# Kernel tuning notes

Measured on AMD Instinct MI355X. Metric: run time of the kernel, lower is better.

Reference implementation:

```python
import jax, jax.numpy as jnp
import numpy as np

B, C, H, W = 8, 128, 64, 64
NWIN, HEADS, QKDIM, KVPW, TOPK = 8, 8, 128, 4, 16
SCALE = QKDIM ** -0.5

def _ln(x, g, b, eps):
    mu = x.mean(-1, keepdims=True)
    var = ((x - mu) ** 2).mean(-1, keepdims=True)
    return (x - mu) * jax.lax.rsqrt(var + eps) * g + b

def _conv(x, w, b, pad, groups=1):
    y = jax.lax.conv_general_dilated(x, w, (1, 1), [(pad, pad), (pad, pad)],
        dimension_numbers=('NCHW', 'OIHW', 'NCHW'), feature_group_count=groups)
    return y + b[None, :, None, None]

def setup_inputs():
    key = jax.random.key(0)
    ks = jax.random.split(key, 8)
    s = 0.05
    return {
        't1': jax.random.normal(ks[0], (B, C, H, W), jnp.float32),
        't2': jax.random.normal(ks[1], (B, C, H, W), jnp.float32),
        'pos_w': jax.random.normal(ks[2], (C, 1, 3, 3), jnp.float32) * s,
        'pos_b': jnp.zeros((C,), jnp.float32),
        'cat_w': jax.random.normal(ks[3], (C, 2 * C, 3, 3), jnp.float32) * s,
        'cat_b': jnp.zeros((C,), jnp.float32),
        'ln_cat_g': jnp.ones((C,), jnp.float32),
        'ln_cat_b': jnp.zeros((C,), jnp.float32),
        'ln1_g': jnp.ones((C,), jnp.float32),
        'ln1_b': jnp.zeros((C,), jnp.float32),
        'qkv_w': jax.random.normal(ks[4], (2 * QKDIM + C, C), jnp.float32) * s,
        'qkv_b': jnp.zeros((2 * QKDIM + C,), jnp.float32),
        'lepe_w': jax.random.normal(ks[5], (C, 1, 5, 5), jnp.float32) * s,
        'lepe_b': jnp.zeros((C,), jnp.float32),
        'wo_w': jax.random.normal(ks[6], (C, C), jnp.float32) * s,
        'wo_b': jnp.zeros((C,), jnp.float32),
    }

def _bra_cross(q_in, kv_in, qkv_w, qkv_b, lepe_w, lepe_b, wo_w, wo_b):
    # Bi-level routing cross attention: queries from q_in, keys/values from kv_in (NHWC).
    p = NWIN; wh, ww = H // p, W // p; p2 = p * p
    q = (q_in @ qkv_w.T + qkv_b)[..., :QKDIM]          # (B,H,W,QKDIM)
    kv = (kv_in @ qkv_w.T + qkv_b)[..., QKDIM:]        # (B,H,W,QKDIM+C)

    def win(x):
        c = x.shape[-1]
        return x.reshape(B, p, wh, p, ww, c).transpose(0, 1, 3, 2, 4, 5).reshape(B, p2, wh, ww, c)

    qw, kvw = win(q), win(kv)
    q_pix = qw.reshape(B, p2, wh * ww, QKDIM)
    # adaptive avg-pool each window's kv to KVPW x KVPW ('ada_avgpool')
    f = wh // KVPW
    kv_pix = kvw.reshape(B, p2, KVPW, f, KVPW, f, QKDIM + C).mean(axis=(3, 5))
    kv_pix = kv_pix.reshape(B, p2, KVPW * KVPW, QKDIM + C)
    q_win = qw.mean(axis=(2, 3))                        # (B,p2,QKDIM)
    k_win = kvw[..., :QKDIM].mean(axis=(2, 3))
    # LePE: depthwise 5x5 conv on full-resolution v
    v_full = kv[..., QKDIM:].transpose(0, 3, 1, 2)
    lepe = _conv(v_full, lepe_w, lepe_b, 2, groups=C).transpose(0, 2, 3, 1)
    # region-level routing (detached: diff_routing=False)
    logits = jnp.einsum('bpc,bqc->bpq',
                        jax.lax.stop_gradient(q_win) * SCALE,
                        jax.lax.stop_gradient(k_win))
    _, r_idx = jax.lax.top_k(logits, TOPK)              # (B,p2,TOPK)
    # gather kv of routed regions: (B,p2,TOPK,KVPW^2,QKDIM+C)
    kv_sel = jax.vmap(lambda kvp, idx: kvp[idx])(kv_pix, r_idx)
    k_sel = kv_sel[..., :QKDIM].reshape(B, p2, TOPK * KVPW * KVPW, HEADS, QKDIM // HEADS)
    v_sel = kv_sel[..., QKDIM:].reshape(B, p2, TOPK * KVPW * KVPW, HEADS, C // HEADS)
    q_h = q_pix.reshape(B, p2, wh * ww, HEADS, QKDIM // HEADS)
    attn = jnp.einsum('bpqmc,bpkmc->bpmqk', q_h * SCALE, k_sel)
    attn = jax.nn.softmax(attn, axis=-1)
    out = jnp.einsum('bpmqk,bpkmc->bpqmc', attn, v_sel).reshape(B, p2, wh, ww, C)
    out = out.reshape(B, p, p, wh, ww, C).transpose(0, 1, 3, 2, 4, 5).reshape(B, H, W, C)
    out = out + lepe
    return out @ wo_w.T + wo_b

def reference(t1, t2, pos_w, pos_b, cat_w, cat_b, ln_cat_g, ln_cat_b,
              ln1_g, ln1_b, qkv_w, qkv_b, lepe_w, lepe_b, wo_w, wo_b):
    # Block.forward: depthwise conv positional embedding
    t1 = t1 + _conv(t1, pos_w, pos_b, 1, groups=C)
    t2 = t2 + _conv(t2, pos_w, pos_b, 1, groups=C)
    t1n = t1.transpose(0, 2, 3, 1)
    t2n = t2.transpose(0, 2, 3, 1)
    # RGBConcatConv: cat on channel-last, 3x3 conv, relu(LayerNorm)
    xc = jnp.concatenate([t1n, t2n], axis=3).transpose(0, 3, 1, 2)
    xc = _conv(xc, cat_w, cat_b, 1).transpose(0, 2, 3, 1)
    x = jax.nn.relu(_ln(xc, ln_cat_g, ln_cat_b, 1e-5))
    attn = _bra_cross(_ln(t1n, ln1_g, ln1_b, 1e-6), _ln(t2n, ln1_g, ln1_b, 1e-6),
                      qkv_w, qkv_b, lepe_w, lepe_b, wo_w, wo_b)
    x = x + attn
    return x.transpose(0, 3, 1, 2)
```

## Files before the change

kernel.cpp:

```cpp
#include <hip/hip_runtime.h>
#include <math.h>

typedef unsigned short ushort_t;
typedef __attribute__((ext_vector_type(4))) float f32x4;
typedef __attribute__((ext_vector_type(16))) float f32x16;
typedef __attribute__((ext_vector_type(8))) short bf16x8;

constexpr int B = 8, C = 128, H = 64, W = 64;
constexpr int HEADS = 8, TOPK = 16;
constexpr int P2 = 64;
constexpr float SCALE = 0.0883883476483184405f;

constexpr size_t NPIX    = (size_t)B * H * W;
constexpr size_t OFF_T1C = 0;
constexpr size_t OFF_T2C = OFF_T1C + NPIX * 128;
constexpr size_t OFF_X   = OFF_T2C + NPIX * 128;
constexpr size_t OFF_QB  = OFF_X   + NPIX * 128;
constexpr size_t OFF_KV  = OFF_QB  + NPIX * 64;
constexpr size_t OFF_KVP = OFF_KV  + NPIX * 256;
constexpr size_t OFF_RW1 = OFF_KVP + 524288;
constexpr size_t OFF_RW2 = OFF_RW1 + 524288;
constexpr size_t OFF_KVPT= OFF_KVP + (size_t)B * P2 * 16 * 256;
constexpr size_t OFF_QW  = OFF_KVPT+ (size_t)B * P2 * 128 * 16 / 2;
constexpr size_t OFF_KW  = OFF_QW  + (size_t)B * P2 * 128;
constexpr size_t OFF_RIDX= OFF_KW  + (size_t)B * P2 * 128;
constexpr size_t OFF_WCB = OFF_RIDX+ (size_t)B * P2 * TOPK;
constexpr size_t OFF_QKVB= OFF_WCB + (size_t)9 * 256 * 128;
constexpr size_t OFF_WOB = OFF_QKVB+ (size_t)384 * 128 / 2;
constexpr size_t OFF_T1B = OFF_WOB + 8192;
constexpr size_t OFF_T2B = OFF_T1B + NPIX * 64;

__device__ inline ushort_t f2bf(float f) {
    unsigned u = __float_as_uint(f);
    unsigned r = u + 0x7FFFu + ((u >> 16) & 1u);
    return (ushort_t)(r >> 16);
}
__device__ inline float bf2f(ushort_t u) {
    return __uint_as_float((unsigned)u << 16);
}

__global__ __launch_bounds__(256) void prep_pos_k(
        const float* __restrict__ t1, const float* __restrict__ t2,
        const float* __restrict__ pos_w, const float* __restrict__ pos_b,
        const float* __restrict__ qkv_w, const float* __restrict__ wo_w,
        const float* __restrict__ cat_w,
        ushort_t* __restrict__ qkvB, ushort_t* __restrict__ woB,
        ushort_t* __restrict__ wcat2,
        float* __restrict__ out1, float* __restrict__ out2,
        ushort_t* __restrict__ ob1, ushort_t* __restrict__ ob2) {
    __shared__ float tile[4][32][33];
    int bid = blockIdx.x;
    int t = threadIdx.x;
    if (bid < 1152) {
        int idx = bid * 256 + t;
        if (idx < 384 * 128) qkvB[idx] = f2bf(qkv_w[idx]);
        if (idx < 128 * 128) woB[idx]  = f2bf(wo_w[idx]);
        if (idx < 36 * 8 * 128 * 8) {
            int i  = idx & 7;
            int n  = (idx >> 3) & 127;
            int r  = idx >> 10;
            int lg = r & 3;
            int kk = (r >> 2) & 1;
            int sdd = r >> 3;
            int dd = sdd % 9, q = sdd / 9;
            int ci = q * 64 + kk * 32 + lg * 8 + i;
            wcat2[idx] = f2bf(cat_w[((size_t)n * 256 + ci) * 9 + dd]);
        }
        return;
    }
    int pb = bid - 1152;
    int xb = pb & 1, cg = (pb >> 1) & 3, z = pb >> 3;
    int which = z >> 7, rem = z & 127;
    int b = rem >> 4, y0 = (rem & 15) * 4;
    const float* in = which ? t2 : t1;
    float* outNHWC = which ? out2 : out1;
    ushort_t* outB = which ? ob2 : ob1;
    int c0 = cg * 32, x0 = xb * 32;
    int tx = t & 31, tg = t >> 5;
    int x = x0 + tx;
    for (int i = 0; i < 4; i++) {
        int cl = tg * 4 + i, c = c0 + cl;
        const float* base = in + (size_t)(b * C + c) * H * W;
        float wv[9];
#pragma unroll
        for (int j = 0; j < 9; j++) wv[j] = pos_w[c * 9 + j];
        float rows[6][3];
#pragma unroll
        for (int yy = 0; yy < 6; yy++) {
            int gy = y0 - 1 + yy;
            bool yok = (gy >= 0 && gy < H);
#pragma unroll
            for (int dx = 0; dx < 3; dx++) {
                int gx = x + dx - 1;
                rows[yy][dx] = (yok && gx >= 0 && gx < W) ? base[gy * W + gx] : 0.f;
            }
        }
        float bb = pos_b[c];
#pragma unroll
        for (int k = 0; k < 4; k++) {
            float acc = rows[k + 1][1] + bb;
#pragma unroll
            for (int dy = 0; dy < 3; dy++)
#pragma unroll
                for (int dx = 0; dx < 3; dx++)
                    acc += rows[k + dy][dx] * wv[dy * 3 + dx];
            tile[k][cl][tx] = acc;
        }
    }
    __syncthreads();
    for (int k = 0; k < 4; k++)
        for (int i = 0; i < 4; i++) {
            int xl = tg * 4 + i;
            float val = tile[k][tx][xl];
            size_t idx = ((size_t)(b * H + y0 + k) * W + x0 + xl) * 128 + c0 + tx;
            outNHWC[idx] = val;
            outB[idx] = f2bf(val);
        }
}

constexpr int HALO_B2 = 180 * 144;
constexpr int XSH_B   = 128 * 272;
__global__ __launch_bounds__(512) void cat_ln_k(
        const ushort_t* __restrict__ t1b, const ushort_t* __restrict__ t2b,
        const ushort_t* __restrict__ wcat2,
        const float* __restrict__ cat_b,
        const float* __restrict__ gcat, const float* __restrict__ bcat,
        ushort_t* __restrict__ xbuf,
        const float* __restrict__ t1c, const float* __restrict__ t2c,
        const float* __restrict__ g1, const float* __restrict__ b1,
        const ushort_t* __restrict__ qkvB, const float* __restrict__ qkv_b,
        ushort_t* __restrict__ outQ, ushort_t* __restrict__ outKV,
        float* __restrict__ rw1, float* __restrict__ rw2) {
    __shared__ __align__(16) unsigned char smem[XSH_B + 8192];
    int bid = blockIdx.x;
    int t = threadIdx.x;
    int lane = t & 63, wv = t >> 6;
    int l15 = lane & 15, lg = lane >> 4;

    if (bid < 256) {
        int cb = bid;
        int mw = wv >> 2, nw = wv & 3;
        int b = cb >> 5, y0 = ((cb >> 3) & 3) * 16, x0 = (cb & 7) * 8;

        f32x4 acc[4][2];
#pragma unroll
        for (int mt = 0; mt < 4; mt++)
#pragma unroll
            for (int cf = 0; cf < 2; cf++)
                acc[mt][cf] = (f32x4){0.f, 0.f, 0.f, 0.f};

        int pyA[4], pxA[4];
#pragma unroll
        for (int mt = 0; mt < 4; mt++) {
            int p = mw * 64 + mt * 16 + l15;
            pyA[mt] = p >> 3; pxA[mt] = p & 7;
        }

        for (int q = 0; q < 4; q++) {
            __syncthreads();
            {
                const ushort_t* src = (q < 2 ? t1b : t2b);
                int coff = (q & 1) * 64;
                for (int e = t; e < 1440; e += 512) {
                    int pix = e >> 3, c8 = e & 7;
                    int hy = pix / 10, hx = pix - hy * 10;
                    int gy = y0 - 1 + hy, gx = x0 - 1 + hx;
                    uint4 v = make_uint4(0u, 0u, 0u, 0u);
                    if (gy >= 0 && gy < H && gx >= 0 && gx < W)
                        v = *reinterpret_cast<const uint4*>(
                            src + ((size_t)(b * H + gy) * W + gx) * 128 + coff + c8 * 8);
                    *reinterpret_cast<uint4*>(smem + pix * 144 + c8 * 16) = v;
                }
            }
            __syncthreads();
#pragma unroll
            for (int dd = 0; dd < 9; dd++) {
                int dy = dd / 3, dx = dd - dy * 3;
                const ushort_t* wb = wcat2 + ((size_t)((q * 9 + dd) * 8 + lg) * 128) * 8;
                bf16x8 bfr[2][2];
#pragma unroll
                for (int kk = 0; kk < 2; kk++)
#pragma unroll
                    for (int cf = 0; cf < 2; cf++)
                        bfr[kk][cf] = *reinterpret_cast<const bf16x8*>(
                            wb + (size_t)kk * 4096 + (nw * 32 + cf * 16 + l15) * 8);
#pragma unroll
                for (int mt = 0; mt < 4; mt++) {
                    bf16x8 af[2];
#pragma unroll
                    for (int kk = 0; kk < 2; kk++)
                        af[kk] = *reinterpret_cast<const bf16x8*>(
                            smem + ((pyA[mt] + dy) * 10 + pxA[mt] + dx) * 144 +
                            kk * 64 + lg * 16);
#pragma unroll
                    for (int cf = 0; cf < 2; cf++)
#pragma unroll
                        for (int kk = 0; kk < 2; kk++)
                            acc[mt][cf] = __builtin_amdgcn_mfma_f32_16x16x32_bf16(
                                af[kk], bfr[kk][cf], acc[mt][cf], 0, 0, 0);
                }
            }
        }

        ushort_t* xsh = (ushort_t*)smem;
        float* psum  = (float*)(smem + XSH_B);
        float* psum2 = (float*)(smem + XSH_B + 4096);
        float gv[2], bvv[2];
#pragma unroll
        for (int cf = 0; cf < 2; cf++) {
            int n = nw * 32 + cf * 16 + l15;
            float cbv = cat_b[n];
            gv[cf] = gcat[n]; bvv[cf] = bcat[n];
#pragma unroll
            for (int mt = 0; mt < 4; mt++)
#pragma unroll
                for (int i = 0; i < 4; i++) acc[mt][cf][i] += cbv;
        }
#pragma unroll
        for (int mt = 0; mt < 4; mt++)
#pragma unroll
            for (int i = 0; i < 4; i++) {
                float s = acc[mt][0][i] + acc[mt][1][i];
                float s2 = acc[mt][0][i] * acc[mt][0][i] + acc[mt][1][i] * acc[mt][1][i];
                s  += __shfl_xor(s, 1, 64);  s2 += __shfl_xor(s2, 1, 64);
                s  += __shfl_xor(s, 2, 64);  s2 += __shfl_xor(s2, 2, 64);
                s  += __shfl_xor(s, 4, 64);  s2 += __shfl_xor(s2, 4, 64);
                s  += __shfl_xor(s, 8, 64);  s2 += __shfl_xor(s2, 8, 64);
                int p = mw * 64 + mt * 16 + lg * 4 + i;
                if (l15 == 0) { psum[wv * 128 + p] = s; psum2[wv * 128 + p] = s2; }
            }
        __syncthreads();
#pragma unroll
        for (int mt = 0; mt < 4; mt++)
#pragma unroll
            for (int i = 0; i < 4; i++) {
                int p = mw * 64 + mt * 16 + lg * 4 + i;
                float tot = 0.f, tot2 = 0.f;
#pragma unroll
                for (int j = 0; j < 4; j++) {
                    tot  += psum[(mw * 4 + j) * 128 + p];
                    tot2 += psum2[(mw * 4 + j) * 128 + p];
                }
                float mean = tot * (1.f / 128.f);
                float inv = rsqrtf(tot2 * (1.f / 128.f) - mean * mean + 1e-5f);
#pragma unroll
                for (int cf = 0; cf < 2; cf++) {
                    float v = (acc[mt][cf][i] - mean) * inv * gv[cf] + bvv[cf];
                    xsh[p * 136 + nw * 32 + cf * 16 + l15] = f2bf(fmaxf(v, 0.f));
                }
            }
        __syncthreads();
        for (int e = t; e < 2048; e += 512) {
            int pix = e >> 4, c16 = e & 15;
            int gy = y0 + (pix >> 3), gx = x0 + (pix & 7);
            *reinterpret_cast<uint4*>(
                xbuf + ((size_t)(b * H + gy) * W + gx) * 128 + c16 * 8) =
                *reinterpret_cast<const uint4*>(xsh + pix * 136 + c16 * 8);
        }
        return;
    }

    unsigned char* ash = smem;
    int lb = bid - 256;
    int which = lb >> 8;
    int blk = lb & 255;
    const float* in = which ? t2c : t1c;
    float* rw = which ? rw2 : rw1;
    size_t p0 = (size_t)blk * 128;
    int bb_ = blk >> 5, y0 = (blk & 31) * 2;
    {
        int row = t >> 2, sub = t & 3;
        const float* src = in + (p0 + row) * 128 + sub * 32;
        float4 v[8];
        float s = 0.f;
#pragma unroll
        for (int j = 0; j < 8; j++) {
            v[j] = *reinterpret_cast<const float4*>(src + j * 4);
            s += v[j].x + v[j].y + v[j].z + v[j].w;
        }
        s += __shfl_xor(s, 1, 64); s += __shfl_xor(s, 2, 64);
        float mean = s * (1.f / 128.f);
        float s2 = 0.f;
#pragma unroll
        for (int j = 0; j < 8; j++) {
            float dx = v[j].x - mean, dy = v[j].y - mean;
            float dz = v[j].z - mean, dw = v[j].w - mean;
            s2 += dx * dx + dy * dy + dz * dz + dw * dw;
        }
        s2 += __shfl_xor(s2, 1, 64); s2 += __shfl_xor(s2, 2, 64);
        float inv = rsqrtf(s2 * (1.f / 128.f) + 1e-6f);
        int wj = (wv & 3) * 2 + (lane >> 5);
        int yy_ = y0 + (wv >> 2);
        bool writer = (lane & 28) == 0;
        float* rwp = rw + (((size_t)(bb_ * 8 + wj) * 64 + yy_) * 128) + sub * 32;
#pragma unroll
        for (int j = 0; j < 8; j++) {
            int c = sub * 32 + j * 4;
            float4 gv = *reinterpret_cast<const float4*>(g1 + c);
            float4 bv = *reinterpret_cast<const float4*>(b1 + c);
            float o0 = (v[j].x - mean) * inv * gv.x + bv.x;
            float o1 = (v[j].y - mean) * inv * gv.y + bv.y;
            float o2 = (v[j].z - mean) * inv * gv.z + bv.z;
            float o3 = (v[j].w - mean) * inv * gv.w + bv.w;
            uint2 pk;
            pk.x = (unsigned)f2bf(o0) | ((unsigned)f2bf(o1) << 16);
            pk.y = (unsigned)f2bf(o2) | ((unsigned)f2bf(o3) << 16);
            *reinterpret_cast<uint2*>(ash + row * 272 + c * 2) = pk;
            float r0 = o0, r1 = o1, r2 = o2, r3 = o3;
#pragma unroll
            for (int m = 4; m <= 16; m <<= 1) {
                r0 += __shfl_xor(r0, m, 64);
                r1 += __shfl_xor(r1, m, 64);
                r2 += __shfl_xor(r2, m, 64);
                r3 += __shfl_xor(r3, m, 64);
            }
            if (writer)
                *reinterpret_cast<float4*>(rwp + j * 4) = make_float4(r0, r1, r2, r3);
        }
    }
    __syncthreads();
    int mh = wv >> 2, nw = wv & 3;
    if (which == 0) {
        f32x4 acc[4][2];
#pragma unroll
        for (int mt = 0; mt < 4; mt++)
#pragma unroll
            for (int nn = 0; nn < 2; nn++)
                acc[mt][nn] = (f32x4){0.f, 0.f, 0.f, 0.f};
#pragma unroll
        for (int ks = 0; ks < 4; ks++) {
            bf16x8 af[4];
#pragma unroll
            for (int mt = 0; mt < 4; mt++)
                af[mt] = *reinterpret_cast<const bf16x8*>(
                    ash + (mh * 64 + mt * 16 + l15) * 272 + ks * 64 + lg * 16);
#pragma unroll
            for (int nn = 0; nn < 2; nn++) {
                int n = (nw * 2 + nn) * 16 + l15;
                bf16x8 bfr = *reinterpret_cast<const bf16x8*>(
                    qkvB + (size_t)n * 128 + ks * 32 + lg * 8);
#pragma unroll
                for (int mt = 0; mt < 4; mt++)
                    acc[mt][nn] = __builtin_amdgcn_mfma_f32_16x16x32_bf16(
                        af[mt], bfr, acc[mt][nn], 0, 0, 0);
            }
        }
#pragma unroll
        for (int nn = 0; nn < 2; nn++) {
            int cg = (nw * 2 + nn) * 16 + l15;
            float bv = qkv_b[cg];
#pragma unroll
            for (int mt = 0; mt < 4; mt++)
#pragma unroll
                for (int i = 0; i < 4; i++) {
                    size_t pix = p0 + mh * 64 + mt * 16 + lg * 4 + i;
                    outQ[pix * 128 + cg] = f2bf((acc[mt][nn][i] + bv) * SCALE);
                }
        }
    } else {
        f32x4 acc[4][4];
#pragma unroll
        for (int mt = 0; mt < 4; mt++)
#pragma unroll
            for (int nn = 0; nn < 4; nn++)
                acc[mt][nn] = (f32x4){0.f, 0.f, 0.f, 0.f};
#pragma unroll
        for (int ks = 0; ks < 4; ks++) {
            bf16x8 af[4];
#pragma unroll
            for (int mt = 0; mt < 4; mt++)
                af[mt] = *reinterpret_cast<const bf16x8*>(
                    ash + (mh * 64 + mt * 16 + l15) * 272 + ks * 64 + lg * 16);
#pragma unroll
            for (int nn = 0; nn < 4; nn++) {
                int n = 128 + (nw * 4 + nn) * 16 + l15;
                bf16x8 bfr = *reinterpret_cast<const bf16x8*>(
                    qkvB + (size_t)n * 128 + ks * 32 + lg * 8);
#pragma unroll
                for (int mt = 0; mt < 4; mt++)
                    acc[mt][nn] = __builtin_amdgcn_mfma_f32_16x16x32_bf16(
                        af[mt], bfr, acc[mt][nn], 0, 0, 0);
            }
        }
#pragma unroll
        for (int nn = 0; nn < 4; nn++) {
            int cg = (nw * 4 + nn) * 16 + l15;
            float bv = qkv_b[128 + cg];
#pragma unroll
            for (int mt = 0; mt < 4; mt++)
#pragma unroll
                for (int i = 0; i < 4; i++) {
                    size_t pix = p0 + mh * 64 + mt * 16 + lg * 4 + i;
                    outKV[pix * 256 + cg] = f2bf(acc[mt][nn][i] + bv);
                }
        }
    }
}

__global__ __launch_bounds__(256) void route_pool_k(
        const float* __restrict__ rw1, const float* __restrict__ rw2,
        const float* __restrict__ qkv_w, const float* __restrict__ qkv_b,
        float* __restrict__ qwin, float* __restrict__ kwin,
        const ushort_t* __restrict__ kv,
        ushort_t* __restrict__ kb, ushort_t* __restrict__ kvpT,
        ushort_t* __restrict__ vpl) {
    __shared__ float msh[2][8][128];
    int bid = blockIdx.x;
    int t = threadIdx.x;
    if (bid < 64) {
        int b = bid >> 3, wi = bid & 7;
        for (int i = t; i < 8 * 128; i += 256) {
            int r = i >> 7, c = i & 127;
            size_t off = (((size_t)(b * 8 + r) * 64) + wi * 8) * 128 + c;
            float s1 = 0.f, s2 = 0.f;
#pragma unroll
            for (int rr = 0; rr < 8; rr++) {
                s1 += rw1[off + rr * 128];
                s2 += rw2[off + rr * 128];
            }
            msh[0][r][c] = s1 * (1.f / 64.f);
            msh[1][r][c] = s2 * (1.f / 64.f);
        }
        __syncthreads();
        int c = t;
        int which = c >> 7;
        const float* wrow = qkv_w + (size_t)c * 128;
        float acc[8];
#pragma unroll
        for (int r = 0; r < 8; r++) acc[r] = 0.f;
        for (int k = 0; k < 128; k++) {
            float wv_ = wrow[k];
#pragma unroll
            for (int r = 0; r < 8; r++) acc[r] += msh[which][r][k] * wv_;
        }
        float bv = qkv_b[c];
#pragma unroll
        for (int r = 0; r < 8; r++) {
            size_t o = ((size_t)b * 64 + wi * 8 + r) * 128 + (c & 127);
            (which ? kwin : qwin)[o] = acc[r] + bv;
        }
        return;
    }
    int pb = bid - 64;
    int b = pb >> 6, wdw = pb & 63;
    int wi = wdw >> 3, wj = wdw & 7;
    if (t < 128) {
        float vals[16];
        for (int ry = 0; ry < 4; ry++)
            for (int rx = 0; rx < 4; rx++) {
                float s = 0.f;
                for (int fy = 0; fy < 2; fy++)
                    for (int fx = 0; fx < 2; fx++) {
                        int y = wi * 8 + ry * 2 + fy, x = wj * 8 + rx * 2 + fx;
                        s += bf2f(kv[((size_t)(b * H + y) * W + x) * 256 + t]);
                    }
                vals[ry * 4 + rx] = s * 0.25f;
            }
#pragma unroll
        for (int pos = 0; pos < 16; pos++)
            kb[(((size_t)(b * 64 + wdw)) * 16 + pos) * 128 + t] = f2bf(vals[pos]);
    } else {
        int c = t - 128;
        float ps[4][4];
#pragma unroll
        for (int i = 0; i < 4; i++)
#pragma unroll
            for (int j = 0; j < 4; j++) ps[i][j] = 0.f;
        for (int y = 0; y < 8; y++) {
            union { ushort_t u16[8]; uint4 u4; } raw;
#pragma unroll
            for (int x = 0; x < 8; x++) {
                raw.u16[x] = kv[((size_t)(b * H + wi * 8 + y) * W + wj * 8 + x) * 256 + 128 + c];
                ps[y >> 1][x >> 1] += bf2f(raw.u16[x]);
            }
            *reinterpret_cast<uint4*>(
                vpl + ((size_t)(b * C + c) * H + wi * 8 + y) * W + wj * 8) = raw.u4;
        }
        union { ushort_t u16[16]; uint4 u4[2]; } pk;
#pragma unroll
        for (int ry = 0; ry < 4; ry++)
#pragma unroll
            for (int rx = 0; rx < 4; rx++)
                pk.u16[ry * 4 + rx] = f2bf(ps[ry][rx] * 0.25f);
        size_t base = (((size_t)(b * 64 + wdw)) * 128 + c) * 16;
        *reinterpret_cast<uint4*>(kvpT + base) = pk.u4[0];
        *reinterpret_cast<uint4*>(kvpT + base + 8) = pk.u4[1];
    }
}

__global__ __launch_bounds__(256) void route_lepe_k(
        const float* __restrict__ q_win, const float* __restrict__ k_win,
        int* __restrict__ r_idx,
        const ushort_t* __restrict__ vpl,
        const float* __restrict__ w, const float* __restrict__ bias,
        ushort_t* __restrict__ lep) {
    __shared__ float tile[68][69];
    int bid = blockIdx.x;
    int t = threadIdx.x;
    if (bid < 128) {
        int b = bid >> 4, p = (bid & 15) * 4 + (t >> 6);
        int j = t & 63;
        const float* qp = q_win + (size_t)(b * 64 + p) * 128;
        const float* kp = k_win + (size_t)(b * 64 + j) * 128;
        float lg = 0.f;
        for (int c = 0; c < 128; c++) lg += qp[c] * kp[c];
        lg *= SCALE;
        for (int it = 0; it < TOPK; it++) {
            float v = lg; int idx = j;
#pragma unroll
            for (int m = 32; m > 0; m >>= 1) {
                float ov = __shfl_xor(v, m, 64);
                int   oi = __shfl_xor(idx, m, 64);
                if (ov > v || (ov == v && oi < idx)) { v = ov; idx = oi; }
            }
            if (j == 0) r_idx[(size_t)(b * 64 + p) * TOPK + it] = idx;
            if (j == idx) lg = -__builtin_inff();
        }
        return;
    }
    int lb = bid - 128;
    int c = lb & 127, b = lb >> 7;
    const ushort_t* plane = vpl + (size_t)(b * C + c) * 4096;
    for (int e = t; e < 68 * 68; e += 256) {
        int row = e / 68, col = e - row * 68;
        int gy = row - 2, gx = col - 2;
        tile[row][col] = (gy >= 0 && gy < 64 && gx >= 0 && gx < 64)
                         ? bf2f(plane[gy * 64 + gx]) : 0.f;
    }
    float wv[25];
#pragma unroll
    for (int j = 0; j < 25; j++) wv[j] = w[c * 25 + j];
    float bb = bias[c];
    __syncthreads();
    int y = t >> 2, x0 = (t & 3) * 16;
    float acc[16];
#pragma unroll
    for (int i = 0; i < 16; i++) acc[i] = bb;
#pragma unroll
    for (int dy = 0; dy < 5; dy++) {
        float vals[20];
#pragma unroll
        for (int j = 0; j < 20; j++) vals[j] = tile[y + dy][x0 + j];
#pragma unroll
        for (int dx = 0; dx < 5; dx++)
#pragma unroll
            for (int i = 0; i < 16; i++)
                acc[i] += vals[i + dx] * wv[dy * 5 + dx];
    }
    ushort_t* dst = lep + (size_t)(b * C + c) * 4096 + y * 64 + x0;
    union { ushort_t u16[16]; uint4 u4[2]; } pk;
#pragma unroll
    for (int i = 0; i < 16; i++) pk.u16[i] = f2bf(acc[i]);
    *reinterpret_cast<uint4*>(dst) = pk.u4[0];
    *reinterpret_cast<uint4*>(dst + 8) = pk.u4[1];
}

__global__ __launch_bounds__(256) void attn_mfma_k(
        const ushort_t* __restrict__ qb,
        const ushort_t* __restrict__ kb,
        const ushort_t* __restrict__ kvpT,
        const int* __restrict__ r_idx,
        ushort_t* __restrict__ o) {
    __shared__ int ridx_sh[16];
    __shared__ float denom_sh[4][32];
    __shared__ __align__(16) ushort_t osh[64][32];

    int b = blockIdx.z, p = blockIdx.x, pair = blockIdx.y;
    int wi = p >> 3, wj = p & 7;
    int t = threadIdx.x;
    int lane = t & 63, wv = t >> 6;
    int l31 = lane & 31, hi = lane >> 5;

    if (t < 16) ridx_sh[t] = r_idx[(size_t)(b * 64 + p) * TOPK + t];
    __syncthreads();

    int hh = wv >> 1, qt = wv & 1;
    int h = pair * 2 + hh;

    int q = qt * 32 + l31;
    int qy = wi * 8 + (q >> 3), qx = wj * 8 + (q & 7);
    bf16x8 qf = *reinterpret_cast<const bf16x8*>(
        qb + ((size_t)(b * H + qy) * W + qx) * 128 + h * 16 + hi * 8);

    const ushort_t* kb_b = kb + (size_t)b * 64 * 16 * 128 + h * 16 + hi * 8;
    const ushort_t* vt_b = kvpT + (size_t)b * 64 * 128 * 16 + (h * 16 + (l31 & 15)) * 16 + hi * 8;

    float m_run = -INFINITY, l_run = 0.f;
    f32x16 opv;
#pragma unroll
    for (int r = 0; r < 16; r++) opv[r] = 0.f;
    f32x16 zf;
#pragma unroll
    for (int r = 0; r < 16; r++) zf[r] = 0.f;

    bf16x8 kf = *reinterpret_cast<const bf16x8*>(
        kb_b + ((size_t)ridx_sh[l31 >> 4] * 16 + (l31 & 15)) * 128);
    bf16x8 v0 = *reinterpret_cast<const bf16x8*>(vt_b + (size_t)ridx_sh[0] * 2048);
    bf16x8 v1 = *reinterpret_cast<const bf16x8*>(vt_b + (size_t)ridx_sh[1] * 2048);

    for (int t8 = 0; t8 < 8; t8++) {
        bf16x8 kfn = kf, v0n = v0, v1n = v1;
        if (t8 < 7) {
            kfn = *reinterpret_cast<const bf16x8*>(
                kb_b + ((size_t)ridx_sh[2 * t8 + 2 + (l31 >> 4)] * 16 + (l31 & 15)) * 128);
            v0n = *reinterpret_cast<const bf16x8*>(vt_b + (size_t)ridx_sh[2 * t8 + 2] * 2048);
            v1n = *reinterpret_cast<const bf16x8*>(vt_b + (size_t)ridx_sh[2 * t8 + 3] * 2048);
        }
        f32x16 S = __builtin_amdgcn_mfma_f32_32x32x16_bf16(kf, qf, zf, 0, 0, 0);
        float tm = S[0];
#pragma unroll
        for (int r = 1; r < 16; r++) tm = fmaxf(tm, S[r]);
        tm = fmaxf(tm, __shfl_xor(tm, 32, 64));
        float m_new = fmaxf(m_run, tm);
        float corr = __expf(m_run - m_new);
        float p_[16], psum = 0.f;
#pragma unroll
        for (int r = 0; r < 16; r++) { p_[r] = __expf(S[r] - m_new); psum += p_[r]; }
        psum += __shfl_xor(psum, 32, 64);
        l_run = l_run * corr + psum;
        m_run = m_new;
#pragma unroll
        for (int r = 0; r < 16; r++) opv[r] *= corr;
        unsigned w_[8], pw_[8];
#pragma unroll
        for (int j = 0; j < 8; j++)
            w_[j] = (__float_as_uint(p_[2 * j]) >> 16) |
                    (__float_as_uint(p_[2 * j + 1]) & 0xFFFF0000u);
#pragma unroll
        for (int j = 0; j < 8; j++) pw_[j] = __shfl_xor(w_[j], 32, 64);
        union { unsigned u[4]; bf16x8 v; } fa0, fa1;
        fa0.u[0] = hi ? pw_[2] : w_[0];
        fa0.u[1] = hi ? pw_[3] : w_[1];
        fa0.u[2] = hi ? w_[2]  : pw_[0];
        fa0.u[3] = hi ? w_[3]  : pw_[1];
        fa1.u[0] = hi ? pw_[6] : w_[4];
        fa1.u[1] = hi ? pw_[7] : w_[5];
        fa1.u[2] = hi ? w_[6]  : pw_[4];
        fa1.u[3] = hi ? w_[7]  : pw_[5];
        opv = __builtin_amdgcn_mfma_f32_32x32x16_bf16(fa0.v, v0, opv, 0, 0, 0);
        opv = __builtin_amdgcn_mfma_f32_32x32x16_bf16(fa1.v, v1, opv, 0, 0, 0);
        kf = kfn; v0 = v0n; v1 = v1n;
    }
    denom_sh[wv][l31] = l_run;
    if (l31 < 16) {
#pragma unroll
        for (int r = 0; r < 16; r++) {
            int qr = (r & 3) + 8 * (r >> 2) + 4 * hi;
            float invd = 1.f / denom_sh[wv][qr];
            osh[qt * 32 + qr][hh * 16 + l31] = f2bf(opv[r] * invd);
        }
    }
    __syncthreads();
    {
        int p_ = t >> 2, seg = t & 3;
        int y = wi * 8 + (p_ >> 3), x = wj * 8 + (p_ & 7);
        *reinterpret_cast<uint4*>(
            o + ((size_t)(b * H + y) * W + x) * 128 + pair * 32 + seg * 8) =
            *reinterpret_cast<const uint4*>(&osh[p_][seg * 8]);
    }
}

__global__ __launch_bounds__(256) void epilogue_mfma_k(
        const ushort_t* __restrict__ o,
        const ushort_t* __restrict__ lep,
        const ushort_t* __restrict__ xbuf,
        const ushort_t* __restrict__ woB,
        const float* __restrict__ wo_b,
        float* __restrict__ out) {
    __shared__ __align__(16) unsigned char smem[128 * 68 * 4];
    ushort_t* ash = (ushort_t*)smem;
    float* res = (float*)smem;
    int t = threadIdx.x, lane = t & 63, wv = t >> 6;
    int bid = blockIdx.x;
    int b = bid >> 6, y = bid & 63;
    size_t p0 = (size_t)bid * 64;

#pragma unroll
    for (int k = 0; k < 4; k++) {
        int e = k * 256 + t;
        int c = e >> 3, xg = e & 7;
        union { uint4 u4; ushort_t u16[8]; } v;
        v.u4 = *reinterpret_cast<const uint4*>(
            lep + (((size_t)(b * C + c) * 64 + y) * 64) + xg * 8);
#pragma unroll
        for (int j = 0; j < 8; j++) ash[(xg * 8 + j) * 136 + c] = v.u16[j];
    }
    __syncthreads();
    {
        int x = t >> 2, sub = t & 3;
        const ushort_t* op = o + (p0 + x) * 128 + sub * 32;
        ushort_t* ap = ash + x * 136 + sub * 32;
#pragma unroll
        for (int jj = 0; jj < 4; jj++) {
            union { uint4 u4; ushort_t u16[8]; } ov, lv;
            ov.u4 = *reinterpret_cast<const uint4*>(op + jj * 8);
            lv.u4 = *reinterpret_cast<const uint4*>(ap + jj * 8);
#pragma unroll
            for (int j = 0; j < 8; j++)
                lv.u16[j] = f2bf(bf2f(ov.u16[j]) + bf2f(lv.u16[j]));
            *reinterpret_cast<uint4*>(ap + jj * 8) = lv.u4;
        }
    }
    __syncthreads();
    int l15 = lane & 15, lg = lane >> 4;
    f32x4 acc[4][2];
#pragma unroll
    for (int mt = 0; mt < 4; mt++)
#pragma unroll
        for (int nn = 0; nn < 2; nn++)
            acc[mt][nn] = (f32x4){0.f, 0.f, 0.f, 0.f};
#pragma unroll
    for (int ks = 0; ks < 4; ks++) {
        bf16x8 af[4];
#pragma unroll
        for (int mt = 0; mt < 4; mt++)
            af[mt] = *reinterpret_cast<const bf16x8*>(
                ash + (mt * 16 + l15) * 136 + ks * 32 + lg * 8);
#pragma unroll
        for (int nn = 0; nn < 2; nn++) {
            int n = (wv * 2 + nn) * 16 + l15;
            bf16x8 bfr = *reinterpret_cast<const bf16x8*>(
                woB + (size_t)n * 128 + ks * 32 + lg * 8);
#pragma unroll
            for (int mt = 0; mt < 4; mt++)
                acc[mt][nn] = __builtin_amdgcn_mfma_f32_16x16x32_bf16(
                    af[mt], bfr, acc[mt][nn], 0, 0, 0);
        }
    }
    __syncthreads();
#pragma unroll
    for (int nn = 0; nn < 2; nn++) {
        int n = (wv * 2 + nn) * 16 + l15;
        float wb = wo_b[n];
#pragma unroll
        for (int mt = 0; mt < 4; mt++)
#pragma unroll
            for (int i = 0; i < 4; i++) {
                int r = mt * 16 + lg * 4 + i;
                float xb = bf2f(xbuf[(p0 + r) * 128 + n]);
                res[n * 68 + r] = acc[mt][nn][i] + wb + xb;
            }
    }
    __syncthreads();
    {
        int c = t >> 1, x0 = (t & 1) * 32;
        float* dst = out + ((size_t)(b * C + c) * 64 + y) * 64 + x0;
#pragma unroll
        for (int gblk = 0; gblk < 8; gblk++)
            *reinterpret_cast<float4*>(dst + gblk * 4) =
                *reinterpret_cast<const float4*>(&res[c * 68 + x0 + gblk * 4]);
    }
}

extern "C" void kernel_launch(void* const* d_in, const int* in_sizes, int n_in,
                              void* d_out, int out_size, void* d_ws, size_t ws_size,
                              hipStream_t stream) {
    const float* t1      = (const float*)d_in[0];
    const float* t2      = (const float*)d_in[1];
    const float* pos_w   = (const float*)d_in[2];
    const float* pos_b   = (const float*)d_in[3];
    const float* cat_w   = (const float*)d_in[4];
    const float* cat_b   = (const float*)d_in[5];
    const float* ln_cat_g= (const float*)d_in[6];
    const float* ln_cat_b= (const float*)d_in[7];
    const float* ln1_g   = (const float*)d_in[8];
    const float* ln1_b   = (const float*)d_in[9];
    const float* qkv_w   = (const float*)d_in[10];
    const float* qkv_b   = (const float*)d_in[11];
    const float* lepe_w  = (const float*)d_in[12];
    const float* lepe_b  = (const float*)d_in[13];
    const float* wo_w    = (const float*)d_in[14];
    const float* wo_b    = (const float*)d_in[15];

    float* ws    = (float*)d_ws;
    float* t1c   = ws + OFF_T1C;
    float* t2c   = ws + OFF_T2C;
    ushort_t* xbuf = (ushort_t*)(ws + OFF_X);
    ushort_t* qbuf = (ushort_t*)(ws + OFF_QB);
    ushort_t* kvbuf= (ushort_t*)(ws + OFF_KV);
    ushort_t* kb   = (ushort_t*)(ws + OFF_KVP);
    float* rw1   = ws + OFF_RW1;
    float* rw2   = ws + OFF_RW2;
    ushort_t* kvpT = (ushort_t*)(ws + OFF_KVPT);
    float* qwin  = ws + OFF_QW;
    float* kwin  = ws + OFF_KW;
    int*   ridx  = (int*)(ws + OFF_RIDX);
    ushort_t* wcat2 = (ushort_t*)(ws + OFF_WCB);
    ushort_t* qkvB  = (ushort_t*)(ws + OFF_QKVB);
    ushort_t* woB   = (ushort_t*)(ws + OFF_WOB);
    ushort_t* t1b   = (ushort_t*)(ws + OFF_T1B);
    ushort_t* t2b   = (ushort_t*)(ws + OFF_T2B);
    ushort_t* obuf  = (ushort_t*)(ws + OFF_T1C);
    ushort_t* vpl   = (ushort_t*)(ws + OFF_T2C);
    ushort_t* lep   = (ushort_t*)(ws + OFF_KV);
    float* out   = (float*)d_out;

    prep_pos_k<<<3200, 256, 0, stream>>>(
        t1, t2, pos_w, pos_b, qkv_w, wo_w, cat_w,
        qkvB, woB, wcat2, t1c, t2c, t1b, t2b);
    cat_ln_k<<<768, 512, 0, stream>>>(
        t1b, t2b, wcat2, cat_b, ln_cat_g, ln_cat_b, xbuf,
        t1c, t2c, ln1_g, ln1_b, qkvB, qkv_b, qbuf, kvbuf, rw1, rw2);
    route_pool_k<<<576, 256, 0, stream>>>(
        rw1, rw2, qkv_w, qkv_b, qwin, kwin, kvbuf, kb, kvpT, vpl);
    route_lepe_k<<<1152, 256, 0, stream>>>(
        qwin, kwin, ridx, vpl, lepe_w, lepe_b, lep);
    attn_mfma_k<<<dim3(64, 4, B), 256, 0, stream>>>(qbuf, kb, kvpT, ridx, obuf);
    epilogue_mfma_k<<<512, 256, 0, stream>>>(obuf, lep, xbuf, woB, wo_b, out);
}
```

Measured before the change: 159.6 us.

## Move LePE depthwise conv from routing kernel into attention kernel launch

Splits the old route+LePE kernel so routing runs alone in a small launch. The LePE 5x5 depthwise conv blocks now share a launch with the attention MFMA blocks, picked by block index. The aim is to overlap the memory-bound conv with the compute-heavy attention and to keep the routing kernel from being slowed by LePE work. The cost is one shared-memory buffer sized for the larger branch, which may lower attention-block occupancy. Block count stays at six launches.

```diff
diff --git a/kernel.cpp b/kernel.cpp
--- a/kernel.cpp
+++ b/kernel.cpp
@@ -118,7 +118,6 @@
         }
 }
 
-constexpr int HALO_B2 = 180 * 144;
 constexpr int XSH_B   = 128 * 272;
 __global__ __launch_bounds__(512) void cat_ln_k(
         const ushort_t* __restrict__ t1b, const ushort_t* __restrict__ t2b,
@@ -488,37 +487,145 @@
     }
 }
 
-__global__ __launch_bounds__(256) void route_lepe_k(
+__global__ __launch_bounds__(256) void route_k(
         const float* __restrict__ q_win, const float* __restrict__ k_win,
-        int* __restrict__ r_idx,
-        const ushort_t* __restrict__ vpl,
-        const float* __restrict__ w, const float* __restrict__ bias,
-        ushort_t* __restrict__ lep) {
-    __shared__ float tile[68][69];
+        int* __restrict__ r_idx) {
     int bid = blockIdx.x;
     int t = threadIdx.x;
-    if (bid < 128) {
-        int b = bid >> 4, p = (bid & 15) * 4 + (t >> 6);
-        int j = t & 63;
-        const float* qp = q_win + (size_t)(b * 64 + p) * 128;
-        const float* kp = k_win + (size_t)(b * 64 + j) * 128;
-        float lg = 0.f;
-        for (int c = 0; c < 128; c++) lg += qp[c] * kp[c];
-        lg *= SCALE;
-        for (int it = 0; it < TOPK; it++) {
-            float v = lg; int idx = j;
-#pragma unroll
-            for (int m = 32; m > 0; m >>= 1) {
-                float ov = __shfl_xor(v, m, 64);
-                int   oi = __shfl_xor(idx, m, 64);
-                if (ov > v || (ov == v && oi < idx)) { v = ov; idx = oi; }
-            }
-            if (j == 0) r_idx[(size_t)(b * 64 + p) * TOPK + it] = idx;
-            if (j == idx) lg = -__builtin_inff();
+    int b = bid >> 4, p = (bid & 15) * 4 + (t >> 6);
+    int j = t & 63;
+    const float* qp = q_win + (size_t)(b * 64 + p) * 128;
+    const float* kp = k_win + (size_t)(b * 64 + j) * 128;
+    float lg = 0.f;
+    for (int c = 0; c < 128; c++) lg += qp[c] * kp[c];
+    lg *= SCALE;
+    for (int it = 0; it < TOPK; it++) {
+        float v = lg; int idx = j;
+#pragma unroll
+        for (int m = 32; m > 0; m >>= 1) {
+            float ov = __shfl_xor(v, m, 64);
+            int   oi = __shfl_xor(idx, m, 64);
+            if (ov > v || (ov == v && oi < idx)) { v = ov; idx = oi; }
+        }
+        if (j == 0) r_idx[(size_t)(b * 64 + p) * TOPK + it] = idx;
+        if (j == idx) lg = -__builtin_inff();
+    }
+}
+
+__global__ __launch_bounds__(256) void attn_lepe_k(
+        const ushort_t* __restrict__ qb,
+        const ushort_t* __restrict__ kb,
+        const ushort_t* __restrict__ kvpT,
+        const int* __restrict__ r_idx,
+        ushort_t* __restrict__ o,
+        const ushort_t* __restrict__ vpl,
+        const float* __restrict__ lw, const float* __restrict__ lbias,
+        ushort_t* __restrict__ lep) {
+    __shared__ __align__(16) unsigned char smem[68 * 69 * 4];
+    int bid = blockIdx.x;
+    int t = threadIdx.x;
+
+    if (bid < 2048) {
+        int* ridx_sh = (int*)smem;
+        float* denom_sh = (float*)(smem + 64);
+        ushort_t* osh = (ushort_t*)(smem + 64 + 512);
+        int p = bid & 63, pair = (bid >> 6) & 3, b = bid >> 8;
+        int wi = p >> 3, wj = p & 7;
+        int lane = t & 63, wv = t >> 6;
+        int l31 = lane & 31, hi = lane >> 5;
+
+        if (t < 16) ridx_sh[t] = r_idx[(size_t)(b * 64 + p) * TOPK + t];
+        __syncthreads();
+
+        int hh = wv >> 1, qt = wv & 1;
+        int h = pair * 2 + hh;
+
+        int q = qt * 32 + l31;
+        int qy = wi * 8 + (q >> 3), qx = wj * 8 + (q & 7);
+        bf16x8 qf = *reinterpret_cast<const bf16x8*>(
+            qb + ((size_t)(b * H + qy) * W + qx) * 128 + h * 16 + hi * 8);
+
+        const ushort_t* kb_b = kb + (size_t)b * 64 * 16 * 128 + h * 16 + hi * 8;
+        const ushort_t* vt_b = kvpT + (size_t)b * 64 * 128 * 16 + (h * 16 + (l31 & 15)) * 16 + hi * 8;
+
+        float m_run = -INFINITY, l_run = 0.f;
+        f32x16 opv;
+#pragma unroll
+        for (int r = 0; r < 16; r++) opv[r] = 0.f;
+        f32x16 zf;
+#pragma unroll
+        for (int r = 0; r < 16; r++) zf[r] = 0.f;
+
+        bf16x8 kf = *reinterpret_cast<const bf16x8*>(
+            kb_b + ((size_t)ridx_sh[l31 >> 4] * 16 + (l31 & 15)) * 128);
+        bf16x8 v0 = *reinterpret_cast<const bf16x8*>(vt_b + (size_t)ridx_sh[0] * 2048);
+        bf16x8 v1 = *reinterpret_cast<const bf16x8*>(vt_b + (size_t)ridx_sh[1] * 2048);
+
+        for (int t8 = 0; t8 < 8; t8++) {
+            bf16x8 kfn = kf, v0n = v0, v1n = v1;
+            if (t8 < 7) {
+                kfn = *reinterpret_cast<const bf16x8*>(
+                    kb_b + ((size_t)ridx_sh[2 * t8 + 2 + (l31 >> 4)] * 16 + (l31 & 15)) * 128);
+                v0n = *reinterpret_cast<const bf16x8*>(vt_b + (size_t)ridx_sh[2 * t8 + 2] * 2048);
+                v1n = *reinterpret_cast<const bf16x8*>(vt_b + (size_t)ridx_sh[2 * t8 + 3] * 2048);
+            }
+            f32x16 S = __builtin_amdgcn_mfma_f32_32x32x16_bf16(kf, qf, zf, 0, 0, 0);
+            float tm = S[0];
+#pragma unroll
+            for (int r = 1; r < 16; r++) tm = fmaxf(tm, S[r]);
+            tm = fmaxf(tm, __shfl_xor(tm, 32, 64));
+            float m_new = fmaxf(m_run, tm);
+            float corr = __expf(m_run - m_new);
+            float p_[16], psum = 0.f;
+#pragma unroll
+            for (int r = 0; r < 16; r++) { p_[r] = __expf(S[r] - m_new); psum += p_[r]; }
+            psum += __shfl_xor(psum, 32, 64);
+            l_run = l_run * corr + psum;
+            m_run = m_new;
+#pragma unroll
+            for (int r = 0; r < 16; r++) opv[r] *= corr;
+            unsigned w_[8], pw_[8];
+#pragma unroll
+            for (int j = 0; j < 8; j++)
+                w_[j] = (__float_as_uint(p_[2 * j]) >> 16) |
+                        (__float_as_uint(p_[2 * j + 1]) & 0xFFFF0000u);
+#pragma unroll
+            for (int j = 0; j < 8; j++) pw_[j] = __shfl_xor(w_[j], 32, 64);
+            union { unsigned u[4]; bf16x8 v; } fa0, fa1;
+            fa0.u[0] = hi ? pw_[2] : w_[0];
+            fa0.u[1] = hi ? pw_[3] : w_[1];
+            fa0.u[2] = hi ? w_[2]  : pw_[0];
+            fa0.u[3] = hi ? w_[3]  : pw_[1];
+            fa1.u[0] = hi ? pw_[6] : w_[4];
+            fa1.u[1] = hi ? pw_[7] : w_[5];
+            fa1.u[2] = hi ? w_[6]  : pw_[4];
+            fa1.u[3] = hi ? w_[7]  : pw_[5];
+            opv = __builtin_amdgcn_mfma_f32_32x32x16_bf16(fa0.v, v0, opv, 0, 0, 0);
+            opv = __builtin_amdgcn_mfma_f32_32x32x16_bf16(fa1.v, v1, opv, 0, 0, 0);
+            kf = kfn; v0 = v0n; v1 = v1n;
+        }
+        denom_sh[wv * 32 + l31] = l_run;
+        if (l31 < 16) {
+#pragma unroll
+            for (int r = 0; r < 16; r++) {
+                int qr = (r & 3) + 8 * (r >> 2) + 4 * hi;
+                float invd = 1.f / denom_sh[wv * 32 + qr];
+                osh[(qt * 32 + qr) * 32 + hh * 16 + l31] = f2bf(opv[r] * invd);
+            }
+        }
+        __syncthreads();
+        {
+            int p_ = t >> 2, seg = t & 3;
+            int y = wi * 8 + (p_ >> 3), x = wj * 8 + (p_ & 7);
+            *reinterpret_cast<uint4*>(
+                o + ((size_t)(b * H + y) * W + x) * 128 + pair * 32 + seg * 8) =
+                *reinterpret_cast<const uint4*>(&osh[p_ * 32 + seg * 8]);
         }
         return;
     }
-    int lb = bid - 128;
+
+    float (*tile)[69] = (float(*)[69])smem;
+    int lb = bid - 2048;
     int c = lb & 127, b = lb >> 7;
     const ushort_t* plane = vpl + (size_t)(b * C + c) * 4096;
     for (int e = t; e < 68 * 68; e += 256) {
@@ -529,8 +636,8 @@
     }
     float wv[25];
 #pragma unroll
-    for (int j = 0; j < 25; j++) wv[j] = w[c * 25 + j];
-    float bb = bias[c];
+    for (int j = 0; j < 25; j++) wv[j] = lw[c * 25 + j];
+    float bb = lbias[c];
     __syncthreads();
     int y = t >> 2, x0 = (t & 3) * 16;
     float acc[16];
@@ -553,111 +660,6 @@
     for (int i = 0; i < 16; i++) pk.u16[i] = f2bf(acc[i]);
     *reinterpret_cast<uint4*>(dst) = pk.u4[0];
     *reinterpret_cast<uint4*>(dst + 8) = pk.u4[1];
-}
-
-__global__ __launch_bounds__(256) void attn_mfma_k(
-        const ushort_t* __restrict__ qb,
-        const ushort_t* __restrict__ kb,
-        const ushort_t* __restrict__ kvpT,
-        const int* __restrict__ r_idx,
-        ushort_t* __restrict__ o) {
-    __shared__ int ridx_sh[16];
-    __shared__ float denom_sh[4][32];
-    __shared__ __align__(16) ushort_t osh[64][32];
-
-    int b = blockIdx.z, p = blockIdx.x, pair = blockIdx.y;
-    int wi = p >> 3, wj = p & 7;
-    int t = threadIdx.x;
-    int lane = t & 63, wv = t >> 6;
-    int l31 = lane & 31, hi = lane >> 5;
-
-    if (t < 16) ridx_sh[t] = r_idx[(size_t)(b * 64 + p) * TOPK + t];
-    __syncthreads();
-
-    int hh = wv >> 1, qt = wv & 1;
-    int h = pair * 2 + hh;
-
-    int q = qt * 32 + l31;
-    int qy = wi * 8 + (q >> 3), qx = wj * 8 + (q & 7);
-    bf16x8 qf = *reinterpret_cast<const bf16x8*>(
-        qb + ((size_t)(b * H + qy) * W + qx) * 128 + h * 16 + hi * 8);
-
-    const ushort_t* kb_b = kb + (size_t)b * 64 * 16 * 128 + h * 16 + hi * 8;
-    const ushort_t* vt_b = kvpT + (size_t)b * 64 * 128 * 16 + (h * 16 + (l31 & 15)) * 16 + hi * 8;
-
-    float m_run = -INFINITY, l_run = 0.f;
-    f32x16 opv;
-#pragma unroll
-    for (int r = 0; r < 16; r++) opv[r] = 0.f;
-    f32x16 zf;
-#pragma unroll
-    for (int r = 0; r < 16; r++) zf[r] = 0.f;
-
-    bf16x8 kf = *reinterpret_cast<const bf16x8*>(
-        kb_b + ((size_t)ridx_sh[l31 >> 4] * 16 + (l31 & 15)) * 128);
-    bf16x8 v0 = *reinterpret_cast<const bf16x8*>(vt_b + (size_t)ridx_sh[0] * 2048);
-    bf16x8 v1 = *reinterpret_cast<const bf16x8*>(vt_b + (size_t)ridx_sh[1] * 2048);
-
-    for (int t8 = 0; t8 < 8; t8++) {
-        bf16x8 kfn = kf, v0n = v0, v1n = v1;
-        if (t8 < 7) {
-            kfn = *reinterpret_cast<const bf16x8*>(
-                kb_b + ((size_t)ridx_sh[2 * t8 + 2 + (l31 >> 4)] * 16 + (l31 & 15)) * 128);
-            v0n = *reinterpret_cast<const bf16x8*>(vt_b + (size_t)ridx_sh[2 * t8 + 2] * 2048);
-            v1n = *reinterpret_cast<const bf16x8*>(vt_b + (size_t)ridx_sh[2 * t8 + 3] * 2048);
-        }
-        f32x16 S = __builtin_amdgcn_mfma_f32_32x32x16_bf16(kf, qf, zf, 0, 0, 0);
-        float tm = S[0];
-#pragma unroll
-        for (int r = 1; r < 16; r++) tm = fmaxf(tm, S[r]);
-        tm = fmaxf(tm, __shfl_xor(tm, 32, 64));
-        float m_new = fmaxf(m_run, tm);
-        float corr = __expf(m_run - m_new);
-        float p_[16], psum = 0.f;
-#pragma unroll
-        for (int r = 0; r < 16; r++) { p_[r] = __expf(S[r] - m_new); psum += p_[r]; }
-        psum += __shfl_xor(psum, 32, 64);
-        l_run = l_run * corr + psum;
-        m_run = m_new;
-#pragma unroll
-        for (int r = 0; r < 16; r++) opv[r] *= corr;
-        unsigned w_[8], pw_[8];
-#pragma unroll
-        for (int j = 0; j < 8; j++)
-            w_[j] = (__float_as_uint(p_[2 * j]) >> 16) |
-                    (__float_as_uint(p_[2 * j + 1]) & 0xFFFF0000u);
-#pragma unroll
-        for (int j = 0; j < 8; j++) pw_[j] = __shfl_xor(w_[j], 32, 64);
-        union { unsigned u[4]; bf16x8 v; } fa0, fa1;
-        fa0.u[0] = hi ? pw_[2] : w_[0];
-        fa0.u[1] = hi ? pw_[3] : w_[1];
-        fa0.u[2] = hi ? w_[2]  : pw_[0];
-        fa0.u[3] = hi ? w_[3]  : pw_[1];
-        fa1.u[0] = hi ? pw_[6] : w_[4];
-        fa1.u[1] = hi ? pw_[7] : w_[5];
-        fa1.u[2] = hi ? w_[6]  : pw_[4];
-        fa1.u[3] = hi ? w_[7]  : pw_[5];
-        opv = __builtin_amdgcn_mfma_f32_32x32x16_bf16(fa0.v, v0, opv, 0, 0, 0);
-        opv = __builtin_amdgcn_mfma_f32_32x32x16_bf16(fa1.v, v1, opv, 0, 0, 0);
-        kf = kfn; v0 = v0n; v1 = v1n;
-    }
-    denom_sh[wv][l31] = l_run;
-    if (l31 < 16) {
-#pragma unroll
-        for (int r = 0; r < 16; r++) {
-            int qr = (r & 3) + 8 * (r >> 2) + 4 * hi;
-            float invd = 1.f / denom_sh[wv][qr];
-            osh[qt * 32 + qr][hh * 16 + l31] = f2bf(opv[r] * invd);
-        }
-    }
-    __syncthreads();
-    {
-        int p_ = t >> 2, seg = t & 3;
-        int y = wi * 8 + (p_ >> 3), x = wj * 8 + (p_ & 7);
-        *reinterpret_cast<uint4*>(
-            o + ((size_t)(b * H + y) * W + x) * 128 + pair * 32 + seg * 8) =
-            *reinterpret_cast<const uint4*>(&osh[p_][seg * 8]);
-    }
 }
 
 __global__ __launch_bounds__(256) void epilogue_mfma_k(
@@ -803,8 +805,8 @@
         t1c, t2c, ln1_g, ln1_b, qkvB, qkv_b, qbuf, kvbuf, rw1, rw2);
     route_pool_k<<<576, 256, 0, stream>>>(
         rw1, rw2, qkv_w, qkv_b, qwin, kwin, kvbuf, kb, kvpT, vpl);
-    route_lepe_k<<<1152, 256, 0, stream>>>(
-        qwin, kwin, ridx, vpl, lepe_w, lepe_b, lep);
-    attn_mfma_k<<<dim3(64, 4, B), 256, 0, stream>>>(qbuf, kb, kvpT, ridx, obuf);
+    route_k<<<128, 256, 0, stream>>>(qwin, kwin, ridx);
+    attn_lepe_k<<<3072, 256, 0, stream>>>(
+        qbuf, kb, kvpT, ridx, obuf, vpl, lepe_w, lepe_b, lep);
     epilogue_mfma_k<<<512, 256, 0, stream>>>(obuf, lep, xbuf, woB, wo_b, out);
 }
```

After: 166.2 us. 1.04x slower.
